# Kernel tuning notes

Hardware: AMD Instinct MI355X
Metric: run time of the kernel (lower is better)

The kernel has to match this reference:

```python
import jax, jax.numpy as jnp
import numpy as np

FMAP = 5
C = 2048
NC = 201  # n_classes + 1


def _conv(x, w, stride, pad):
    return jax.lax.conv_general_dilated(
        x, w, (stride, stride), [(pad, pad), (pad, pad)],
        dimension_numbers=('NCHW', 'OIHW', 'NCHW'))


def _bn(x, g, b, eps=1e-5):
    # training-mode batch norm (batch statistics), as in the torch forward
    m = x.mean((0, 2, 3), keepdims=True)
    v = x.var((0, 2, 3), keepdims=True)
    return (x - m) / jnp.sqrt(v + eps) * g[None, :, None, None] + b[None, :, None, None]


def _grid_sample(img, grid):
    # img [B,C,H,W]; grid [B,K,2] normalized coords (x,y), align_corners=True,
    # bilinear, zero padding -> [B,C,K]
    B, Ch, H, W = img.shape
    gx = (grid[..., 0] + 1.0) * 0.5 * (W - 1)
    gy = (grid[..., 1] + 1.0) * 0.5 * (H - 1)
    x0 = jnp.floor(gx); y0 = jnp.floor(gy)
    x1 = x0 + 1.0; y1 = y0 + 1.0
    wx1 = gx - x0; wx0 = 1.0 - wx1
    wy1 = gy - y0; wy0 = 1.0 - wy1
    imgf = img.reshape(B, Ch, H * W)

    def gather(xi, yi):
        valid = (xi >= 0) & (xi <= W - 1) & (yi >= 0) & (yi <= H - 1)
        xi_ = jnp.clip(xi, 0, W - 1).astype(jnp.int32)
        yi_ = jnp.clip(yi, 0, H - 1).astype(jnp.int32)
        idx = yi_ * W + xi_  # [B,K]
        v = jnp.take_along_axis(imgf, idx[:, None, :], axis=2)  # [B,C,K]
        return v * valid[:, None, :].astype(img.dtype)

    out = (gather(x0, y0) * (wx0 * wy0)[:, None, :]
           + gather(x1, y0) * (wx1 * wy0)[:, None, :]
           + gather(x0, y1) * (wx0 * wy1)[:, None, :]
           + gather(x1, y1) * (wx1 * wy1)[:, None, :])
    return out


def setup_inputs() -> dict:
    key = jax.random.key(0)
    ks = jax.random.split(key, 12)
    B = 8
    return {
        'x': jax.random.normal(ks[0], (B, C, 10, 10), jnp.float32),
        'epoch': 1,
        'flag': 0,
        'conv_last_w': jax.random.normal(ks[1], (C, C, 3, 3), jnp.float32) * 0.02,
        'bn_last_g': jnp.ones((C,), jnp.float32),
        'bn_last_b': jnp.zeros((C,), jnp.float32),
        'loc_w1': jax.random.normal(ks[2], (C, C, 3, 3), jnp.float32) * 0.02,
        'loc_g1': jnp.ones((C,), jnp.float32),
        'loc_b1': jnp.zeros((C,), jnp.float32),
        'loc_w2': jax.random.normal(ks[3], (C, C, 3, 3), jnp.float32) * 0.02,
        'loc_g2': jnp.ones((C,), jnp.float32),
        'loc_b2': jnp.zeros((C,), jnp.float32),
        'fc1_w': jax.random.normal(ks[4], (512, C * 9), jnp.float32) * 0.02,
        'fc2_w': jax.random.normal(ks[5], (4, 512), jnp.float32) * 0.001,
        'conv_stn_w': jax.random.normal(ks[6], (NC, C, 3, 3), jnp.float32) * 0.02,
        'conv_stn_b': jnp.zeros((NC,), jnp.float32),
    }


def reference(x, epoch, flag, conv_last_w, bn_last_g, bn_last_b,
              loc_w1, loc_g1, loc_b1, loc_w2, loc_g2, loc_b2,
              fc1_w, fc2_w, conv_stn_w, conv_stn_b):
    B = x.shape[0]
    # backbone tail: conv_last (s=2, pad=1) + bn_last -> [B,2048,5,5]
    f = _bn(_conv(x, conv_last_w, 2, 1), bn_last_g, bn_last_b)

    # localization network (conv-bn-relu x2, pad=1) -> [B,2048,5,5]
    xs = jax.nn.relu(_bn(_conv(f, loc_w1, 1, 1), loc_g1, loc_b1))
    xs = jax.nn.relu(_bn(_conv(xs, loc_w2, 1, 1), loc_g2, loc_b2))
    xs_p = jnp.pad(xs, ((0, 0), (0, 0), (1, 1), (1, 1)))  # [B,2048,7,7]

    # batched per-cell fc_loc: 25 overlapping 3x3 patches (i outer, j inner)
    patches = jnp.stack([xs_p[:, :, i:i + 3, j:j + 3]
                         for i in range(FMAP) for j in range(FMAP)], axis=1)
    patches = patches.reshape(B, FMAP * FMAP, C * 9)  # (C, kh, kw) flatten order
    h = jax.nn.relu(jnp.einsum('bpf,hf->bph', patches, fc1_w))
    p = jnp.einsum('bph,oh->bpo', h, fc2_w)  # [B,25,4]

    # theta = [[1+p0, 0, p1], [0, 1+p2, p3]]
    zero = jnp.zeros_like(p[..., 0])
    row0 = jnp.stack([1.0 + p[..., 0], zero, p[..., 1]], -1)
    row1 = jnp.stack([zero, 1.0 + p[..., 2], p[..., 3]], -1)
    theta = jnp.stack([row0, row1], -2)  # [B,25,2,3]

    # identity affine grid on padded 7x7 map (align_corners=True), 3x3 windows
    lin = jnp.linspace(-1.0, 1.0, FMAP + 2)
    gxm, gym = jnp.meshgrid(lin, lin, indexing='xy')  # gxm[y,x]=lin[x]
    base = jnp.stack([gxm, gym], -1)  # [7,7,2]
    pos = jnp.stack([base[i:i + 3, j:j + 3]
                     for i in range(FMAP) for j in range(FMAP)], 0)
    pos_h = jnp.concatenate([pos.reshape(25, 9, 2), jnp.ones((25, 9, 1))], -1)

    # transformed sampling grids: pos_hom @ theta^T -> [B,25,9,2]
    grids = jnp.einsum('pkc,bpdc->bpkd', pos_h, theta).reshape(B, 25 * 9, 2)

    # batched grid_sample of padded features, then stitch 25 3x3 tiles -> 15x15
    f_p = jnp.pad(f, ((0, 0), (0, 0), (1, 1), (1, 1)))  # [B,2048,7,7]
    samp = _grid_sample(f_p, grids)  # [B,C,225]
    temp = samp.reshape(B, C, FMAP, FMAP, 3, 3).transpose(0, 1, 2, 4, 3, 5)
    temp = temp.reshape(B, C, 3 * FMAP, 3 * FMAP)  # [B,2048,15,15]

    # conv_stn (k=3, s=3) -> [B,201,5,5]; joint softmax over class x position
    out = _conv(temp, conv_stn_w, 3, 0) + conv_stn_b[None, :, None, None]
    s = jax.nn.softmax(out.reshape(B, -1), axis=1).reshape(B, NC, FMAP, FMAP)
    classif_scores = s.sum((2, 3))  # [B,201]
    return classif_scores, s, theta.reshape(B * 25, 2, 3)
```

## Files before the change

### kernel.cpp

```cpp
#include <hip/hip_runtime.h>
#include <hip/hip_bf16.h>


#define GK 18432
#define GN 200
#define NPAD 256

typedef __attribute__((ext_vector_type(8))) short bf16x8;
typedef __attribute__((ext_vector_type(4))) float f32x4;
typedef unsigned int u32;

__global__ __launch_bounds__(256) void im2col_bf16(
    const float* __restrict__ in, __hip_bfloat16* __restrict__ Bt,
    int H, int stride, int pad)
{
    int tid = blockIdx.x * 256 + threadIdx.x;
    int n = tid / GK;
    int k = tid - n * GK;
    float v = 0.f;
    if (n < GN) {
        int c = k / 9; int r9 = k - c * 9;
        int kh = r9 / 3, kw = r9 - kh * 3;
        int b = n / 25; int pp = n - b * 25;
        int oh = pp / 5, ow = pp - oh * 5;
        int r = oh * stride + kh - pad;
        int s = ow * stride + kw - pad;
        if (r >= 0 && r < H && s >= 0 && s < H)
            v = in[(((b * 2048 + c) * H) + r) * H + s];
    }
    Bt[tid] = __float2bfloat16(v);
}

__global__ __launch_bounds__(256) void gridsample_bf16(
    const float* __restrict__ f, const float* __restrict__ gridb,
    __hip_bfloat16* __restrict__ Bt)
{
    int tid = blockIdx.x * 256 + threadIdx.x;
    int n = tid / GK;
    int cq = tid - n * GK;
    float v = 0.f;
    if (n < GN) {
        int c = cq / 9, q = cq - c * 9;
        int b = n / 25, p = n - b * 25;
        int g = (b * 225 + p * 9 + q) * 2;
        float px = gridb[g], py = gridb[g + 1];
        float x0f = floorf(px), y0f = floorf(py);
        int x0 = (int)x0f, y0 = (int)y0f;
        float wx1 = px - x0f, wx0 = 1.f - wx1;
        float wy1 = py - y0f, wy0 = 1.f - wy1;
        const float* fb = f + ((size_t)b * 2048 + c) * 25;
        auto fetch = [&](int xi, int yi) -> float {
            if (xi < 1 || xi > 5 || yi < 1 || yi > 5) return 0.f;
            return fb[(yi - 1) * 5 + (xi - 1)];
        };
        v = fetch(x0, y0) * wx0 * wy0
          + fetch(x0 + 1, y0) * wx1 * wy0
          + fetch(x0, y0 + 1) * wx0 * wy1
          + fetch(x0 + 1, y0 + 1) * wx1 * wy1;
    }
    Bt[tid] = __float2bfloat16(v);
}

__global__ __launch_bounds__(256, 2) void gemm_mfma(
    const float* __restrict__ A, const __hip_bfloat16* __restrict__ Bt,
    float* __restrict__ C, int M, int kchunk)
{
    __shared__ unsigned short Bs[2][256 * 32];

    const int tid  = threadIdx.x;
    const int wave = tid >> 6, lane = tid & 63;
    const int lm = lane & 15, lq = lane >> 4;
    const int bm = blockIdx.y * 128;
    const int kbase = blockIdx.z * kchunk;
    const int wm = wave * 32;

    const int koff = (((tid & 3) ^ ((tid >> 3) & 3)) << 3);
    const __hip_bfloat16* bsrc = Bt + (size_t)(tid >> 2) * GK + kbase + koff;
    const int xk = lq ^ ((lm >> 1) & 3);

    int r0 = bm + wm + lm;      if (r0 > M - 1) r0 = M - 1;
    int r1 = bm + wm + 16 + lm; if (r1 > M - 1) r1 = M - 1;
    const float* ap0 = A + (size_t)r0 * GK + kbase + lq * 8;
    const float* ap1 = A + (size_t)r1 * GK + kbase + lq * 8;

    f32x4 acc[2][13] = {};
    const int NS = kchunk >> 5;

    auto stageB = [&](int buf, int k0) {
        unsigned short* dst = &Bs[buf][tid * 8];
        const __hip_bfloat16* s = bsrc + k0;
#pragma unroll
        for (int r = 0; r < 4; ++r)
            __builtin_amdgcn_global_load_lds((const u32*)(s + (size_t)r * 64 * GK),
                                             (u32*)(dst + r * 2048), 16, 0, 0);
    };

    stageB(0, 0);
    float4 ar00 = *(const float4*)(ap0 + 0);
    float4 ar01 = *(const float4*)(ap0 + 4);
    float4 ar10 = *(const float4*)(ap1 + 0);
    float4 ar11 = *(const float4*)(ap1 + 4);

    int cur = 0;
    for (int t = 0; t < NS; ++t) {
        const int kn = (t + 1 < NS) ? ((t + 1) << 5) : (t << 5);
        stageB(cur ^ 1, kn);
        float4 an00 = *(const float4*)(ap0 + kn);
        float4 an01 = *(const float4*)(ap0 + kn + 4);
        float4 an10 = *(const float4*)(ap1 + kn);
        float4 an11 = *(const float4*)(ap1 + kn + 4);

        union { bf16x8 v; u32 u[4]; } af0, af1;
        af0.u[0] = __builtin_amdgcn_perm(__float_as_uint(ar00.y), __float_as_uint(ar00.x), 0x07060302u);
        af0.u[1] = __builtin_amdgcn_perm(__float_as_uint(ar00.w), __float_as_uint(ar00.z), 0x07060302u);
        af0.u[2] = __builtin_amdgcn_perm(__float_as_uint(ar01.y), __float_as_uint(ar01.x), 0x07060302u);
        af0.u[3] = __builtin_amdgcn_perm(__float_as_uint(ar01.w), __float_as_uint(ar01.z), 0x07060302u);
        af1.u[0] = __builtin_amdgcn_perm(__float_as_uint(ar10.y), __float_as_uint(ar10.x), 0x07060302u);
        af1.u[1] = __builtin_amdgcn_perm(__float_as_uint(ar10.w), __float_as_uint(ar10.z), 0x07060302u);
        af1.u[2] = __builtin_amdgcn_perm(__float_as_uint(ar11.y), __float_as_uint(ar11.x), 0x07060302u);
        af1.u[3] = __builtin_amdgcn_perm(__float_as_uint(ar11.w), __float_as_uint(ar11.z), 0x07060302u);

        asm volatile("s_waitcnt vmcnt(8)" ::: "memory");
        __builtin_amdgcn_s_barrier();

#pragma unroll
        for (int j = 0; j < 13; ++j) {
            bf16x8 b = *(const bf16x8*)&Bs[cur][(j * 16 + lm) * 32 + xk * 8];
            acc[0][j] = __builtin_amdgcn_mfma_f32_16x16x32_bf16(af0.v, b, acc[0][j], 0, 0, 0);
            acc[1][j] = __builtin_amdgcn_mfma_f32_16x16x32_bf16(af1.v, b, acc[1][j], 0, 0, 0);
        }

        asm volatile("" ::: "memory");
        __builtin_amdgcn_s_barrier();

        ar00 = an00; ar01 = an01; ar10 = an10; ar11 = an11;
        cur ^= 1;
    }

#pragma unroll
    for (int i = 0; i < 2; ++i) {
        int row0 = bm + wm + i * 16 + lq * 4;
#pragma unroll
        for (int j = 0; j < 13; ++j) {
            int col = j * 16 + lm;
            if (col < GN) {
#pragma unroll
                for (int r = 0; r < 4; ++r) {
                    int row = row0 + r;
                    if (row < M)
                        atomicAdd(&C[(size_t)row * GN + col], acc[i][j][r]);
                }
            }
        }
    }
}

__global__ void bnstats_kernel(const float* __restrict__ y,
                               float* __restrict__ meanb,
                               float* __restrict__ rstdb)
{
    int ch = blockIdx.x;
    int lane = threadIdx.x;
    const float* p = y + (size_t)ch * GN;
    float s = 0.f, sq = 0.f;
    for (int idx = lane; idx < GN; idx += 64) {
        float v = p[idx];
        s += v; sq += v * v;
    }
    for (int off = 32; off; off >>= 1) {
        s += __shfl_down(s, off);
        sq += __shfl_down(sq, off);
    }
    if (lane == 0) {
        float m = s * (1.f / 200.f);
        float var = sq * (1.f / 200.f) - m * m;
        meanb[ch] = m;
        rstdb[ch] = rsqrtf(var + 1e-5f);
    }
}

__global__ __launch_bounds__(256) void bn_apply_kernel(
    const float* __restrict__ y, const float* __restrict__ meanb,
    const float* __restrict__ rstdb, const float* __restrict__ g,
    const float* __restrict__ bb, float* __restrict__ out, int relu)
{
    int tid = blockIdx.x * 256 + threadIdx.x;
    if (tid >= 409600) return;
    int b = tid / (2048 * 25);
    int rem = tid % (2048 * 25);
    int c = rem / 25;
    int pp = rem % 25;
    float v = y[(size_t)c * GN + b * 25 + pp];
    v = (v - meanb[c]) * rstdb[c] * g[c] + bb[c];
    if (relu) v = fmaxf(v, 0.f);
    out[tid] = v;
}

__global__ void fc2_kernel(const float* __restrict__ hmat,
                           const float* __restrict__ fc2w,
                           float* __restrict__ pbuf)
{
    int n = blockIdx.x;
    int oo = threadIdx.x >> 6;
    int lane = threadIdx.x & 63;
    float s = 0.f;
#pragma unroll
    for (int j = 0; j < 8; ++j) {
        int hh = lane + 64 * j;
        s += fmaxf(hmat[(size_t)hh * GN + n], 0.f) * fc2w[oo * 512 + hh];
    }
    for (int off = 32; off; off >>= 1) s += __shfl_down(s, off);
    if (lane == 0) pbuf[n * 4 + oo] = s;
}

__global__ void theta_grids_kernel(const float* __restrict__ pbuf,
                                   float* __restrict__ gridb,
                                   float* __restrict__ outT)
{
    int tid = blockIdx.x * 256 + threadIdx.x;
    if (tid >= 1800) return;
    int b = tid / 225;
    int rem = tid % 225;
    int p = rem / 9;
    int k = rem % 9;
    int i = p / 5, j = p % 5;
    int dy = k / 3, dx = k % 3;
    int n = b * 25 + p;
    float p0 = pbuf[n * 4 + 0];
    float p1 = pbuf[n * 4 + 1];
    float p2 = pbuf[n * 4 + 2];
    float p3 = pbuf[n * 4 + 3];
    float x = (float)(j + dx) * (1.f / 3.f) - 1.f;
    float y = (float)(i + dy) * (1.f / 3.f) - 1.f;
    float gx = (1.f + p0) * x + p1;
    float gy = (1.f + p2) * y + p3;
    gridb[tid * 2 + 0] = (gx + 1.f) * 3.f;
    gridb[tid * 2 + 1] = (gy + 1.f) * 3.f;
    if (k == 0) {
        outT[n * 6 + 0] = 1.f + p0;
        outT[n * 6 + 1] = 0.f;
        outT[n * 6 + 2] = p1;
        outT[n * 6 + 3] = 0.f;
        outT[n * 6 + 4] = 1.f + p2;
        outT[n * 6 + 5] = p3;
    }
}

__global__ void softmax_kernel(const float* __restrict__ stn,
                               const float* __restrict__ bias,
                               float* __restrict__ outC,
                               float* __restrict__ outS)
{
    int b = blockIdx.x;
    __shared__ float red[256];
    int t = threadIdx.x;

    float mx = -1e30f;
    for (int idx = t; idx < 5025; idx += 256) {
        int o = idx / 25, pp = idx % 25;
        mx = fmaxf(mx, stn[(size_t)o * GN + b * 25 + pp] + bias[o]);
    }
    red[t] = mx; __syncthreads();
    for (int s = 128; s; s >>= 1) {
        if (t < s) red[t] = fmaxf(red[t], red[t + s]);
        __syncthreads();
    }
    mx = red[0]; __syncthreads();

    float sm = 0.f;
    for (int idx = t; idx < 5025; idx += 256) {
        int o = idx / 25, pp = idx % 25;
        sm += expf(stn[(size_t)o * GN + b * 25 + pp] + bias[o] - mx);
    }
    red[t] = sm; __syncthreads();
    for (int s = 128; s; s >>= 1) {
        if (t < s) red[t] += red[t + s];
        __syncthreads();
    }
    float inv = 1.f / red[0];

    for (int idx = t; idx < 5025; idx += 256) {
        int o = idx / 25, pp = idx % 25;
        outS[b * 5025 + idx] =
            expf(stn[(size_t)o * GN + b * 25 + pp] + bias[o] - mx) * inv;
    }
    for (int o = t; o < 201; o += 256) {
        float cs = 0.f;
        for (int pp = 0; pp < 25; ++pp)
            cs += expf(stn[(size_t)o * GN + b * 25 + pp] + bias[o] - mx);
        outC[b * 201 + o] = cs * inv;
    }
}

extern "C" void kernel_launch(void* const* d_in, const int* in_sizes, int n_in,
                              void* d_out, int out_size, void* d_ws, size_t ws_size,
                              hipStream_t stream)
{
    const float* x           = (const float*)d_in[0];
    const float* conv_last_w = (const float*)d_in[3];
    const float* bn_last_g   = (const float*)d_in[4];
    const float* bn_last_b   = (const float*)d_in[5];
    const float* loc_w1      = (const float*)d_in[6];
    const float* loc_g1      = (const float*)d_in[7];
    const float* loc_b1      = (const float*)d_in[8];
    const float* loc_w2      = (const float*)d_in[9];
    const float* loc_g2      = (const float*)d_in[10];
    const float* loc_b2      = (const float*)d_in[11];
    const float* fc1_w       = (const float*)d_in[12];
    const float* fc2_w       = (const float*)d_in[13];
    const float* conv_stn_w  = (const float*)d_in[14];
    const float* conv_stn_b  = (const float*)d_in[15];

    __hip_bfloat16* Bt = (__hip_bfloat16*)d_ws;
    float* fp    = (float*)((char*)d_ws + (size_t)NPAD * GK * 2);
    float* t1    = fp;
    float* fbuf  = t1 + 409600;
    float* xs1   = fbuf + 409600;
    float* xs    = xs1 + 409600;
    float* hmat  = xs + 409600;
    float* stn   = hmat + 102400;
    float* pbuf  = stn + 40200;
    float* gridb = pbuf + 800;
    float* meanb = gridb + 3600;
    float* rstdb = meanb + 2048;

    float* outC = (float*)d_out;
    float* outS = outC + 8 * 201;
    float* outT = outS + 8 * 201 * 25;

    dim3 b256(256);
    const int nB = (NPAD * GK) / 256;

    im2col_bf16<<<nB, b256, 0, stream>>>(x, Bt, 10, 2, 1);
    hipMemsetAsync(t1, 0, 409600 * sizeof(float), stream);
    gemm_mfma<<<dim3(1, 16, 16), b256, 0, stream>>>(conv_last_w, Bt, t1, 2048, GK / 16);
    bnstats_kernel<<<2048, 64, 0, stream>>>(t1, meanb, rstdb);
    bn_apply_kernel<<<1600, b256, 0, stream>>>(t1, meanb, rstdb, bn_last_g, bn_last_b, fbuf, 0);

    im2col_bf16<<<nB, b256, 0, stream>>>(fbuf, Bt, 5, 1, 1);
    hipMemsetAsync(t1, 0, 409600 * sizeof(float), stream);
    gemm_mfma<<<dim3(1, 16, 16), b256, 0, stream>>>(loc_w1, Bt, t1, 2048, GK / 16);
    bnstats_kernel<<<2048, 64, 0, stream>>>(t1, meanb, rstdb);
    bn_apply_kernel<<<1600, b256, 0, stream>>>(t1, meanb, rstdb, loc_g1, loc_b1, xs1, 1);

    im2col_bf16<<<nB, b256, 0, stream>>>(xs1, Bt, 5, 1, 1);
    hipMemsetAsync(t1, 0, 409600 * sizeof(float), stream);
    gemm_mfma<<<dim3(1, 16, 16), b256, 0, stream>>>(loc_w2, Bt, t1, 2048, GK / 16);
    bnstats_kernel<<<2048, 64, 0, stream>>>(t1, meanb, rstdb);
    bn_apply_kernel<<<1600, b256, 0, stream>>>(t1, meanb, rstdb, loc_g2, loc_b2, xs, 1);

    im2col_bf16<<<nB, b256, 0, stream>>>(xs, Bt, 5, 1, 1);
    hipMemsetAsync(hmat, 0, 102400 * sizeof(float), stream);
    gemm_mfma<<<dim3(1, 4, 64), b256, 0, stream>>>(fc1_w, Bt, hmat, 512, GK / 64);

    fc2_kernel<<<200, 256, 0, stream>>>(hmat, fc2_w, pbuf);
    theta_grids_kernel<<<8, 256, 0, stream>>>(pbuf, gridb, outT);

    gridsample_bf16<<<nB, b256, 0, stream>>>(fbuf, gridb, Bt);

    hipMemsetAsync(stn, 0, 40200 * sizeof(float), stream);
    gemm_mfma<<<dim3(1, 2, 64), b256, 0, stream>>>(conv_stn_w, Bt, stn, 201, GK / 64);

    softmax_kernel<<<8, 256, 0, stream>>>(stn, conv_stn_b, outC, outS);
}
```

Baseline: 761.1 us.

## Triple-buffer GEMM B tiles, halve M tile per block, raise wave priority

The bf16 MFMA GEMM moves from double to triple buffering of the B tile in LDS, so loads run two stages ahead. The loop is unrolled by three with a relaxed vmcnt wait. Each block now covers 64 rows instead of 128 (one 16-row tile per wave), and the grids double to launch more blocks for latency hiding. s_setprio is raised around the MFMA section. In exchange, B tiles are read from LDS and global memory more often per FLOP, LDS use grows to three buffers, and NS must be divisible by three.

```diff
diff --git a/kernel.cpp b/kernel.cpp
--- a/kernel.cpp
+++ b/kernel.cpp
@@ -65,29 +65,25 @@
     const float* __restrict__ A, const __hip_bfloat16* __restrict__ Bt,
     float* __restrict__ C, int M, int kchunk)
 {
-    __shared__ unsigned short Bs[2][256 * 32];
+    __shared__ unsigned short Bs[3][256 * 32];
 
     const int tid  = threadIdx.x;
     const int wave = tid >> 6, lane = tid & 63;
     const int lm = lane & 15, lq = lane >> 4;
-    const int bm = blockIdx.y * 128;
+    const int bm = blockIdx.y * 64;
     const int kbase = blockIdx.z * kchunk;
-    const int wm = wave * 32;
 
     const int koff = (((tid & 3) ^ ((tid >> 3) & 3)) << 3);
     const __hip_bfloat16* bsrc = Bt + (size_t)(tid >> 2) * GK + kbase + koff;
     const int xk = lq ^ ((lm >> 1) & 3);
 
-    int r0 = bm + wm + lm;      if (r0 > M - 1) r0 = M - 1;
-    int r1 = bm + wm + 16 + lm; if (r1 > M - 1) r1 = M - 1;
-    const float* ap0 = A + (size_t)r0 * GK + kbase + lq * 8;
-    const float* ap1 = A + (size_t)r1 * GK + kbase + lq * 8;
-
-    f32x4 acc[2][13] = {};
+    int r0 = bm + wave * 16 + lm; if (r0 > M - 1) r0 = M - 1;
+    const float* ap = A + (size_t)r0 * GK + kbase + lq * 8;
+
+    f32x4 acc[13] = {};
     const int NS = kchunk >> 5;
 
-    auto stageB = [&](int buf, int k0) {
-        unsigned short* dst = &Bs[buf][tid * 8];
+    auto stageB = [&](unsigned short* dst, int k0) {
         const __hip_bfloat16* s = bsrc + k0;
 #pragma unroll
         for (int r = 0; r < 4; ++r)
@@ -95,61 +91,55 @@
                                              (u32*)(dst + r * 2048), 16, 0, 0);
     };
 
-    stageB(0, 0);
-    float4 ar00 = *(const float4*)(ap0 + 0);
-    float4 ar01 = *(const float4*)(ap0 + 4);
-    float4 ar10 = *(const float4*)(ap1 + 0);
-    float4 ar11 = *(const float4*)(ap1 + 4);
-
-    int cur = 0;
-    for (int t = 0; t < NS; ++t) {
-        const int kn = (t + 1 < NS) ? ((t + 1) << 5) : (t << 5);
-        stageB(cur ^ 1, kn);
-        float4 an00 = *(const float4*)(ap0 + kn);
-        float4 an01 = *(const float4*)(ap0 + kn + 4);
-        float4 an10 = *(const float4*)(ap1 + kn);
-        float4 an11 = *(const float4*)(ap1 + kn + 4);
-
-        union { bf16x8 v; u32 u[4]; } af0, af1;
-        af0.u[0] = __builtin_amdgcn_perm(__float_as_uint(ar00.y), __float_as_uint(ar00.x), 0x07060302u);
-        af0.u[1] = __builtin_amdgcn_perm(__float_as_uint(ar00.w), __float_as_uint(ar00.z), 0x07060302u);
-        af0.u[2] = __builtin_amdgcn_perm(__float_as_uint(ar01.y), __float_as_uint(ar01.x), 0x07060302u);
-        af0.u[3] = __builtin_amdgcn_perm(__float_as_uint(ar01.w), __float_as_uint(ar01.z), 0x07060302u);
-        af1.u[0] = __builtin_amdgcn_perm(__float_as_uint(ar10.y), __float_as_uint(ar10.x), 0x07060302u);
-        af1.u[1] = __builtin_amdgcn_perm(__float_as_uint(ar10.w), __float_as_uint(ar10.z), 0x07060302u);
-        af1.u[2] = __builtin_amdgcn_perm(__float_as_uint(ar11.y), __float_as_uint(ar11.x), 0x07060302u);
-        af1.u[3] = __builtin_amdgcn_perm(__float_as_uint(ar11.w), __float_as_uint(ar11.z), 0x07060302u);
-
-        asm volatile("s_waitcnt vmcnt(8)" ::: "memory");
-        __builtin_amdgcn_s_barrier();
-
+    float4 a00, a01, a10, a11, a20, a21;
+    stageB(&Bs[0][tid * 8], 0);
+    a00 = *(const float4*)(ap + 0);
+    a01 = *(const float4*)(ap + 4);
+    stageB(&Bs[1][tid * 8], 32);
+    a10 = *(const float4*)(ap + 32);
+    a11 = *(const float4*)(ap + 36);
+
+#define GEMM_BODY(RD, ST, CA0, CA1, NA0, NA1, TT)                              \
+    {                                                                          \
+        int kn = (TT) + 2; if (kn >= NS) kn = NS - 1; kn <<= 5;                \
+        stageB(&Bs[ST][tid * 8], kn);                                          \
+        NA0 = *(const float4*)(ap + kn);                                       \
+        NA1 = *(const float4*)(ap + kn + 4);                                   \
+        union { bf16x8 v; u32 u[4]; } af;                                      \
+        af.u[0] = __builtin_amdgcn_perm(__float_as_uint(CA0.y), __float_as_uint(CA0.x), 0x07060302u); \
+        af.u[1] = __builtin_amdgcn_perm(__float_as_uint(CA0.w), __float_as_uint(CA0.z), 0x07060302u); \
+        af.u[2] = __builtin_amdgcn_perm(__float_as_uint(CA1.y), __float_as_uint(CA1.x), 0x07060302u); \
+        af.u[3] = __builtin_amdgcn_perm(__float_as_uint(CA1.w), __float_as_uint(CA1.z), 0x07060302u); \
+        asm volatile("s_waitcnt vmcnt(12)" ::: "memory");                      \
+        __builtin_amdgcn_s_barrier();                                          \
+        __builtin_amdgcn_s_setprio(1);                                         \
+        _Pragma("unroll")                                                      \
+        for (int j = 0; j < 13; ++j) {                                         \
+            bf16x8 b = *(const bf16x8*)&Bs[RD][(j * 16 + lm) * 32 + xk * 8];   \
+            acc[j] = __builtin_amdgcn_mfma_f32_16x16x32_bf16(af.v, b, acc[j], 0, 0, 0); \
+        }                                                                      \
+        __builtin_amdgcn_s_setprio(0);                                         \
+        asm volatile("" ::: "memory");                                         \
+        __builtin_amdgcn_s_barrier();                                          \
+    }
+
+    for (int t = 0; t < NS; t += 3) {
+        GEMM_BODY(0, 2, a00, a01, a20, a21, t);
+        GEMM_BODY(1, 0, a10, a11, a00, a01, t + 1);
+        GEMM_BODY(2, 1, a20, a21, a10, a11, t + 2);
+    }
+#undef GEMM_BODY
+
+    const int orow = bm + wave * 16 + lq * 4;
 #pragma unroll
-        for (int j = 0; j < 13; ++j) {
-            bf16x8 b = *(const bf16x8*)&Bs[cur][(j * 16 + lm) * 32 + xk * 8];
-            acc[0][j] = __builtin_amdgcn_mfma_f32_16x16x32_bf16(af0.v, b, acc[0][j], 0, 0, 0);
-            acc[1][j] = __builtin_amdgcn_mfma_f32_16x16x32_bf16(af1.v, b, acc[1][j], 0, 0, 0);
-        }
-
-        asm volatile("" ::: "memory");
-        __builtin_amdgcn_s_barrier();
-
-        ar00 = an00; ar01 = an01; ar10 = an10; ar11 = an11;
-        cur ^= 1;
-    }
-
+    for (int j = 0; j < 13; ++j) {
+        int col = j * 16 + lm;
+        if (col < GN) {
 #pragma unroll
-    for (int i = 0; i < 2; ++i) {
-        int row0 = bm + wm + i * 16 + lq * 4;
-#pragma unroll
-        for (int j = 0; j < 13; ++j) {
-            int col = j * 16 + lm;
-            if (col < GN) {
-#pragma unroll
-                for (int r = 0; r < 4; ++r) {
-                    int row = row0 + r;
-                    if (row < M)
-                        atomicAdd(&C[(size_t)row * GN + col], acc[i][j][r]);
-                }
+            for (int r = 0; r < 4; ++r) {
+                int row = orow + r;
+                if (row < M)
+                    atomicAdd(&C[(size_t)row * GN + col], acc[j][r]);
             }
         }
     }
@@ -333,25 +323,25 @@
 
     im2col_bf16<<<nB, b256, 0, stream>>>(x, Bt, 10, 2, 1);
     hipMemsetAsync(t1, 0, 409600 * sizeof(float), stream);
-    gemm_mfma<<<dim3(1, 16, 16), b256, 0, stream>>>(conv_last_w, Bt, t1, 2048, GK / 16);
+    gemm_mfma<<<dim3(1, 32, 16), b256, 0, stream>>>(conv_last_w, Bt, t1, 2048, GK / 16);
     bnstats_kernel<<<2048, 64, 0, stream>>>(t1, meanb, rstdb);
     bn_apply_kernel<<<1600, b256, 0, stream>>>(t1, meanb, rstdb, bn_last_g, bn_last_b, fbuf, 0);
 
     im2col_bf16<<<nB, b256, 0, stream>>>(fbuf, Bt, 5, 1, 1);
     hipMemsetAsync(t1, 0, 409600 * sizeof(float), stream);
-    gemm_mfma<<<dim3(1, 16, 16), b256, 0, stream>>>(loc_w1, Bt, t1, 2048, GK / 16);
+    gemm_mfma<<<dim3(1, 32, 16), b256, 0, stream>>>(loc_w1, Bt, t1, 2048, GK / 16);
     bnstats_kernel<<<2048, 64, 0, stream>>>(t1, meanb, rstdb);
     bn_apply_kernel<<<1600, b256, 0, stream>>>(t1, meanb, rstdb, loc_g1, loc_b1, xs1, 1);
 
     im2col_bf16<<<nB, b256, 0, stream>>>(xs1, Bt, 5, 1, 1);
     hipMemsetAsync(t1, 0, 409600 * sizeof(float), stream);
-    gemm_mfma<<<dim3(1, 16, 16), b256, 0, stream>>>(loc_w2, Bt, t1, 2048, GK / 16);
+    gemm_mfma<<<dim3(1, 32, 16), b256, 0, stream>>>(loc_w2, Bt, t1, 2048, GK / 16);
     bnstats_kernel<<<2048, 64, 0, stream>>>(t1, meanb, rstdb);
     bn_apply_kernel<<<1600, b256, 0, stream>>>(t1, meanb, rstdb, loc_g2, loc_b2, xs, 1);
 
     im2col_bf16<<<nB, b256, 0, stream>>>(xs, Bt, 5, 1, 1);
     hipMemsetAsync(hmat, 0, 102400 * sizeof(float), stream);
-    gemm_mfma<<<dim3(1, 4, 64), b256, 0, stream>>>(fc1_w, Bt, hmat, 512, GK / 64);
+    gemm_mfma<<<dim3(1, 8, 64), b256, 0, stream>>>(fc1_w, Bt, hmat, 512, GK / 64);
 
     fc2_kernel<<<200, 256, 0, stream>>>(hmat, fc2_w, pbuf);
     theta_grids_kernel<<<8, 256, 0, stream>>>(pbuf, gridb, outT);
@@ -359,7 +349,7 @@
     gridsample_bf16<<<nB, b256, 0, stream>>>(fbuf, gridb, Bt);
 
     hipMemsetAsync(stn, 0, 40200 * sizeof(float), stream);
-    gemm_mfma<<<dim3(1, 2, 64), b256, 0, stream>>>(conv_stn_w, Bt, stn, 201, GK / 64);
+    gemm_mfma<<<dim3(1, 4, 96), b256, 0, stream>>>(conv_stn_w, Bt, stn, 201, GK / 96);
 
     softmax_kernel<<<8, 256, 0, stream>>>(stn, conv_stn_b, outC, outS);
 }
```

After: 772.8 us. Within noise of the previous version (+1.5%).
